# Kernel optimization log

Hardware: AMD Instinct MI355X
Metric: run time of the kernel (lower is better)

Reference implementation:

```python
import jax, jax.numpy as jnp
import numpy as np

SEQ, BATCH, D, N = 256, 4, 512, 32768
TEMP = 0.5


def setup_inputs() -> dict:
    key = jax.random.key(0)
    ks = jax.random.split(key, 16)
    d = D
    # xavier_uniform with gain 1/sqrt(2) for square [d,d]: limit = gain*sqrt(6/(d+d))
    lim_t = (1.0 / np.sqrt(2.0)) * np.sqrt(6.0 / (d + d))
    lim_g1 = np.sqrt(6.0 / (2 * d + d))  # default kaiming-ish scale approximated by xavier
    lim_g2 = np.sqrt(6.0 / (d + 1))
    inp = {
        "q": jax.random.normal(ks[0], (SEQ, BATCH, D), dtype=jnp.float32),
        "prev_layer_output": jax.random.normal(ks[1], (SEQ, BATCH, D), dtype=jnp.float32),
        "Wq": jax.random.uniform(ks[2], (D, D), jnp.float32, -lim_t, lim_t),
        "bq": jnp.zeros((D,), jnp.float32),
        "Wk": jax.random.uniform(ks[3], (D, D), jnp.float32, -lim_t, lim_t),
        "bk": jnp.zeros((D,), jnp.float32),
        "Wv": jax.random.uniform(ks[4], (D, D), jnp.float32, -lim_t, lim_t),
        "bv": jnp.zeros((D,), jnp.float32),
        "Wg1": jax.random.uniform(ks[5], (D, 2 * D), jnp.float32, -lim_g1, lim_g1),
        "bg1": jnp.zeros((D,), jnp.float32),
        "Wg2": jax.random.uniform(ks[6], (1, D), jnp.float32, -lim_g2, lim_g2),
        "bg2": jnp.zeros((1,), jnp.float32),
        "dstore_k": jax.random.normal(ks[7], (N, D), dtype=jnp.float32),
        "dstore_v": jax.random.normal(ks[8], (N, D), dtype=jnp.float32),
    }
    return inp


def reference(q, prev_layer_output, Wq, bq, Wk, bk, Wv, bv, Wg1, bg1, Wg2, bg2, dstore_k, dstore_v):
    # [S,B,D] -> [B,S,D]
    qb = jnp.transpose(q, (1, 0, 2))
    prevb = jnp.transpose(prev_layer_output, (1, 0, 2))
    # enable_tune projections
    _q = qb @ Wq.T + bq                      # [B,S,D]
    _k = dstore_k @ Wk.T + bk                # [N,D]
    _v = dstore_v @ Wv.T + bv                # [N,D]
    _q = _q * (D ** -0.5)
    # attention over datastore, temperature-scaled softmax
    logits = jnp.einsum("bsd,nd->bsn", _q, _k) / TEMP  # [B,S,N]
    w = jax.nn.softmax(logits, axis=-1)
    attn = jnp.einsum("bsn,nd->bsd", w, _v)            # [B,S,D]
    # gated residual fusion
    cat = jnp.concatenate([attn, prevb], axis=-1)      # [B,S,2D]
    h = jax.nn.relu(cat @ Wg1.T + bg1)                 # [B,S,D]
    sigma = jax.nn.sigmoid(h @ Wg2.T + bg2)            # [B,S,1]
    res = attn * sigma + prevb * (1.0 - sigma)
    return jnp.transpose(res, (1, 0, 2))               # [S,B,D]
```

## Files before the change

kernel.cpp:

```cpp
#include <hip/hip_runtime.h>
#include <hip/hip_bf16.h>
#include <cstdint>
#include <cstddef>


typedef unsigned short u16;
typedef u16    u16x8 __attribute__((ext_vector_type(8)));
typedef u16    u16x4 __attribute__((ext_vector_type(4)));
typedef __bf16 bf16x8 __attribute__((ext_vector_type(8)));
typedef float  f32x4 __attribute__((ext_vector_type(4)));

#define MFMA16(a, b, c) __builtin_amdgcn_mfma_f32_16x16x32_bf16( \
    __builtin_bit_cast(bf16x8, (a)), __builtin_bit_cast(bf16x8, (b)), (c), 0, 0, 0)

__device__ __forceinline__ u16 f2bf(float f) {
  unsigned u = __builtin_bit_cast(unsigned, f);
  u += 0x7fffu + ((u >> 16) & 1u);
  return (u16)(u >> 16);
}

__global__ __launch_bounds__(256) void prep_cvt(const float* __restrict__ src,
                                                u16* __restrict__ dst) {
  size_t i = ((size_t)blockIdx.x * 256 + threadIdx.x) * 4;
  float4 v = *(const float4*)(src + i);
  u16x4 o = {f2bf(v.x), f2bf(v.y), f2bf(v.z), f2bf(v.w)};
  *(u16x4*)(dst + i) = o;
}

__global__ __launch_bounds__(256) void prep_vt(const float* __restrict__ v,
                                               u16* __restrict__ vt) {
  __shared__ u16 Lt[64 * 72];
  const int n0 = blockIdx.x * 64, d0 = blockIdx.y * 64;
  const int t = threadIdx.x;
  const int n = t >> 2, c4 = t & 3;
#pragma unroll
  for (int i = 0; i < 4; i++) {
    int col = (c4 + 4 * i) * 4;
    float4 x = *(const float4*)(v + (size_t)(n0 + n) * 512 + d0 + col);
    Lt[(col + 0) * 72 + n] = f2bf(x.x);
    Lt[(col + 1) * 72 + n] = f2bf(x.y);
    Lt[(col + 2) * 72 + n] = f2bf(x.z);
    Lt[(col + 3) * 72 + n] = f2bf(x.w);
  }
  __syncthreads();
#pragma unroll
  for (int u = 0; u < 2; u++) {
    int unit = t + 256 * u;
    int d = unit >> 3, un = unit & 7;
    *(u16x8*)(vt + (size_t)(d0 + d) * 32768 + n0 + un * 8) =
        *(const u16x8*)&Lt[d * 72 + un * 8];
  }
}

template <bool TRANSB, bool CONCAT, bool RELU, bool OUTBF16, bool ROWSCALE>
__global__ __launch_bounds__(256, 2) void gemm64(
    const float* __restrict__ A, const float* __restrict__ A2,
    const float* __restrict__ B, const float* __restrict__ bias,
    const float* __restrict__ lvec, float alpha, void* __restrict__ Cv,
    int M, int N, int K) {
  __shared__ u16 As[64 * 72];
  __shared__ u16 Bs[64 * 72];
  const int tid = threadIdx.x;
  const int w = tid >> 6, lane = tid & 63, quad = lane >> 4, l15 = lane & 15;
  const int m0 = blockIdx.y * 64, n0 = blockIdx.x * 64;
  const int arow = tid >> 2, ac4 = tid & 3;
  float rs = 1.0f;
  if (ROWSCALE) rs = 1.0f / lvec[m0 + arow];
  const f32x4 fzero = {0.f, 0.f, 0.f, 0.f};
  f32x4 acc[4];
#pragma unroll
  for (int i = 0; i < 4; i++) acc[i] = fzero;

  for (int k0 = 0; k0 < K; k0 += 64) {
    __syncthreads();
    {
      const float* src;
      if (CONCAT)
        src = (k0 < 512) ? (A + (size_t)(m0 + arow) * 512 + k0)
                         : (A2 + (size_t)(m0 + arow) * 512 + (k0 - 512));
      else
        src = A + (size_t)(m0 + arow) * K + k0;
#pragma unroll
      for (int i = 0; i < 4; i++) {
        int col = (ac4 + 4 * i) * 4;
        float4 x = *(const float4*)(src + col);
        if (ROWSCALE) { x.x *= rs; x.y *= rs; x.z *= rs; x.w *= rs; }
        u16x4 o = {f2bf(x.x), f2bf(x.y), f2bf(x.z), f2bf(x.w)};
        *(u16x4*)&As[arow * 72 + col] = o;
      }
    }
    if (TRANSB) {
      const float* src = B + (size_t)(n0 + arow) * K + k0;
#pragma unroll
      for (int i = 0; i < 4; i++) {
        int col = (ac4 + 4 * i) * 4;
        float4 x = *(const float4*)(src + col);
        u16x4 o = {f2bf(x.x), f2bf(x.y), f2bf(x.z), f2bf(x.w)};
        *(u16x4*)&Bs[arow * 72 + col] = o;
      }
    } else {
      const float* src = B + (size_t)(k0 + arow) * N + n0;
#pragma unroll
      for (int i = 0; i < 4; i++) {
        int col = (ac4 + 4 * i) * 4;
        float4 x = *(const float4*)(src + col);
        Bs[(col + 0) * 72 + arow] = f2bf(x.x);
        Bs[(col + 1) * 72 + arow] = f2bf(x.y);
        Bs[(col + 2) * 72 + arow] = f2bf(x.z);
        Bs[(col + 3) * 72 + arow] = f2bf(x.w);
      }
    }
    __syncthreads();
#pragma unroll
    for (int ks = 0; ks < 2; ks++) {
      u16x8 af = *(const u16x8*)&As[(w * 16 + l15) * 72 + ks * 32 + quad * 8];
#pragma unroll
      for (int nt = 0; nt < 4; nt++) {
        u16x8 bf = *(const u16x8*)&Bs[(nt * 16 + l15) * 72 + ks * 32 + quad * 8];
        acc[nt] = MFMA16(af, bf, acc[nt]);
      }
    }
  }
#pragma unroll
  for (int nt = 0; nt < 4; nt++) {
    int col = n0 + nt * 16 + l15;
    float b = bias ? bias[col] : 0.f;
#pragma unroll
    for (int i = 0; i < 4; i++) {
      int row = m0 + w * 16 + quad * 4 + i;
      float y = (acc[nt][i] + b) * alpha;
      if (RELU) y = fmaxf(y, 0.f);
      if (OUTBF16)
        ((u16*)Cv)[(size_t)row * N + col] = f2bf(y);
      else
        ((float*)Cv)[(size_t)row * N + col] = y;
    }
  }
}

__global__ void cq_kernel(const float* __restrict__ q1,
                          const float* __restrict__ bk,
                          float* __restrict__ cq) {
  int r = blockIdx.x, lane = threadIdx.x;
  float s = 0.f;
#pragma unroll
  for (int k = 0; k < 512; k += 64) s += q1[(size_t)r * 512 + k + lane] * bk[k + lane];
#pragma unroll
  for (int off = 32; off; off >>= 1) s += __shfl_down(s, off, 64);
  if (lane == 0) cq[r] = 2.0f * s;
}

__global__ __launch_bounds__(512, 2) void flash(
    const u16* __restrict__ kbf,
    const u16* __restrict__ vt,
    const u16* __restrict__ q2,
    const float* __restrict__ cq,
    float* __restrict__ racc,
    float* __restrict__ lacc) {
  __shared__ u16 Ks[32 * 520];
  __shared__ u16 Es[64 * 40];
  const int tid = threadIdx.x;
  const int w = tid >> 6, lane = tid & 63, quad = lane >> 4, l15 = lane & 15;
  const int qt = blockIdx.x & 15, ch = blockIdx.x >> 4;
  const int qbase = qt * 64;
  const int qg = w >> 1, nh = w & 1;
  const int colb = w * 64;

  u16x8 qf[16];
  {
    const u16* qp = q2 + (size_t)(qbase + qg * 16 + l15) * 512 + quad * 8;
#pragma unroll
    for (int ks = 0; ks < 16; ks++) qf[ks] = *(const u16x8*)(qp + ks * 32);
  }
  float cq4[4];
#pragma unroll
  for (int i = 0; i < 4; i++) cq4[i] = cq[qbase + qg * 16 + quad * 4 + i];
  float lp[4] = {0.f, 0.f, 0.f, 0.f};
  const f32x4 fzero = {0.f, 0.f, 0.f, 0.f};
  f32x4 acc[4][4];
#pragma unroll
  for (int a = 0; a < 4; a++)
#pragma unroll
    for (int b = 0; b < 4; b++) acc[a][b] = fzero;

  u16x8 st[4];
  u16x8 bvp[4];
  int n0 = ch * 2048;
#pragma unroll
  for (int u = 0; u < 4; u++) {
    int flat = tid + u * 512;
    st[u] = *(const u16x8*)(kbf + (size_t)(n0 + (flat >> 6)) * 512 + (flat & 63) * 8);
  }
#pragma unroll
  for (int ct = 0; ct < 4; ct++)
    bvp[ct] = *(const u16x8*)(vt + (size_t)(colb + ct * 16 + l15) * 32768 + n0 + quad * 8);

#pragma unroll 1
  for (int sub = 0; sub < 64; ++sub) {
    n0 = ch * 2048 + sub * 32;
    __syncthreads();
#pragma unroll
    for (int u = 0; u < 4; u++) {
      int flat = tid + u * 512;
      *(u16x8*)&Ks[(flat >> 6) * 520 + (flat & 63) * 8] = st[u];
    }
    if (sub + 1 < 64) {
      int n1 = n0 + 32;
#pragma unroll
      for (int u = 0; u < 4; u++) {
        int flat = tid + u * 512;
        st[u] = *(const u16x8*)(kbf + (size_t)(n1 + (flat >> 6)) * 512 + (flat & 63) * 8);
      }
    }
    __syncthreads();
    f32x4 s = fzero;
#pragma unroll
    for (int ks = 0; ks < 16; ks++) {
      u16x8 bfg = *(const u16x8*)&Ks[(nh * 16 + l15) * 520 + ks * 32 + quad * 8];
      s = MFMA16(qf[ks], bfg, s);
    }
#pragma unroll
    for (int i = 0; i < 4; i++) {
      float e = __expf(s[i] + cq4[i]);
      lp[i] += e;
      Es[(qg * 16 + quad * 4 + i) * 40 + nh * 16 + l15] = f2bf(e);
    }
    __syncthreads();
    u16x8 ef[4];
#pragma unroll
    for (int q2i = 0; q2i < 4; q2i++)
      ef[q2i] = *(const u16x8*)&Es[(q2i * 16 + l15) * 40 + quad * 8];
#pragma unroll
    for (int ct = 0; ct < 4; ct++) {
#pragma unroll
      for (int q2i = 0; q2i < 4; q2i++)
        acc[q2i][ct] = MFMA16(ef[q2i], bvp[ct], acc[q2i][ct]);
    }
    if (sub + 1 < 64) {
      int n1 = n0 + 32;
#pragma unroll
      for (int ct = 0; ct < 4; ct++)
        bvp[ct] = *(const u16x8*)(vt + (size_t)(colb + ct * 16 + l15) * 32768 + n1 + quad * 8);
    }
  }
#pragma unroll
  for (int q2i = 0; q2i < 4; q2i++)
#pragma unroll
    for (int ct = 0; ct < 4; ct++) {
      int col = colb + ct * 16 + l15;
#pragma unroll
      for (int i = 0; i < 4; i++) {
        int row = qbase + q2i * 16 + quad * 4 + i;
        atomicAdd(&racc[(size_t)row * 512 + col], acc[q2i][ct][i]);
      }
    }
#pragma unroll
  for (int i = 0; i < 4; i++) {
    float v = lp[i];
#pragma unroll
    for (int off = 1; off < 16; off <<= 1) v += __shfl_xor(v, off, 64);
    if (l15 == 0) atomicAdd(&lacc[qbase + qg * 16 + quad * 4 + i], v);
  }
}

__global__ __launch_bounds__(256) void finalize(
    const float* __restrict__ h, const float* __restrict__ attn,
    const float* __restrict__ prev, const float* __restrict__ wg2,
    const float* __restrict__ bg2, float* __restrict__ out) {
  __shared__ float red[4];
  int r = blockIdx.x, t = threadIdx.x;
  const float* hr = h + (size_t)r * 512;
  float p = hr[t] * wg2[t] + hr[t + 256] * wg2[t + 256];
#pragma unroll
  for (int off = 32; off; off >>= 1) p += __shfl_down(p, off, 64);
  if ((t & 63) == 0) red[t >> 6] = p;
  __syncthreads();
  float dot = red[0] + red[1] + red[2] + red[3];
  float sg = 1.f / (1.f + __expf(-(dot + bg2[0])));
  size_t base = (size_t)r * 512;
  out[base + t] = attn[base + t] * sg + prev[base + t] * (1.f - sg);
  out[base + t + 256] = attn[base + t + 256] * sg + prev[base + t + 256] * (1.f - sg);
}

extern "C" void kernel_launch(void* const* d_in, const int* in_sizes, int n_in,
                              void* d_out, int out_size, void* d_ws, size_t ws_size,
                              hipStream_t stream) {
  const float* q    = (const float*)d_in[0];
  const float* prev = (const float*)d_in[1];
  const float* Wq   = (const float*)d_in[2];
  const float* bq   = (const float*)d_in[3];
  const float* Wk   = (const float*)d_in[4];
  const float* bk   = (const float*)d_in[5];
  const float* Wv   = (const float*)d_in[6];
  const float* bv   = (const float*)d_in[7];
  const float* Wg1  = (const float*)d_in[8];
  const float* bg1  = (const float*)d_in[9];
  const float* Wg2  = (const float*)d_in[10];
  const float* bg2  = (const float*)d_in[11];
  const float* dk   = (const float*)d_in[12];
  const float* dv   = (const float*)d_in[13];
  float* out = (float*)d_out;

  char* ws = (char*)d_ws;
  u16*   kbf  = (u16*)(ws);
  u16*   vt   = (u16*)(ws + 33554432);
  float* racc = (float*)(ws + 67108864);
  float* lacc = (float*)(ws + 69206016);
  float* cqv  = (float*)(ws + 69210112);
  u16*   q2   = (u16*)(ws + 69214208);
  float* q1   = (float*)(ws + 70262784);
  float* attn = (float*)(ws + 72359936);
  float* h    = q1;

  prep_cvt<<<16384, 256, 0, stream>>>(dk, kbf);
  prep_vt<<<dim3(512, 8), 256, 0, stream>>>(dv, vt);
  gemm64<true, false, false, false, false><<<dim3(8, 16), 256, 0, stream>>>(
      q, nullptr, Wq, bq, nullptr, 0.044194173824159216f, q1, 1024, 512, 512);
  cq_kernel<<<1024, 64, 0, stream>>>(q1, bk, cqv);
  gemm64<false, false, false, true, false><<<dim3(8, 16), 256, 0, stream>>>(
      q1, nullptr, Wk, nullptr, nullptr, 2.0f, q2, 1024, 512, 512);
  hipMemsetAsync(racc, 0, 2097152 + 4096, stream);
  flash<<<256, 512, 0, stream>>>(kbf, vt, q2, cqv, racc, lacc);
  gemm64<true, false, false, false, true><<<dim3(8, 16), 256, 0, stream>>>(
      racc, nullptr, Wv, bv, lacc, 1.0f, attn, 1024, 512, 512);
  gemm64<true, true, true, false, false><<<dim3(8, 16), 256, 0, stream>>>(
      attn, prev, Wg1, bg1, nullptr, 1.0f, h, 1024, 512, 1024);
  finalize<<<1024, 256, 0, stream>>>(h, attn, prev, Wg2, bg2, out);
}
```

Baseline: 419.4 us.

## Fuse cq and gate dot into GEMMs, pipeline flash PV, remap blocks per XCD

```diff
diff --git a/kernel.cpp b/kernel.cpp
--- a/kernel.cpp
+++ b/kernel.cpp
@@ -52,12 +52,14 @@
   }
 }
 
-template <bool TRANSB, bool CONCAT, bool RELU, bool OUTBF16, bool ROWSCALE>
+template <bool TRANSB, bool CONCAT, bool RELU, bool OUTBF16, bool ROWSCALE,
+          bool CQ, bool GATE, int KK>
 __global__ __launch_bounds__(256, 2) void gemm64(
     const float* __restrict__ A, const float* __restrict__ A2,
     const float* __restrict__ B, const float* __restrict__ bias,
-    const float* __restrict__ lvec, float alpha, void* __restrict__ Cv,
-    int M, int N, int K) {
+    const float* __restrict__ lvec, const float* __restrict__ bkv,
+    const float* __restrict__ wg2, float alpha, void* __restrict__ Cv,
+    float* __restrict__ cqout, float* __restrict__ sdot) {
   __shared__ u16 As[64 * 72];
   __shared__ u16 Bs[64 * 72];
   const int tid = threadIdx.x;
@@ -66,49 +68,64 @@
   const int arow = tid >> 2, ac4 = tid & 3;
   float rs = 1.0f;
   if (ROWSCALE) rs = 1.0f / lvec[m0 + arow];
+  const bool docq = CQ && (blockIdx.x == 0);
+  float cqacc = 0.f;
   const f32x4 fzero = {0.f, 0.f, 0.f, 0.f};
   f32x4 acc[4];
 #pragma unroll
   for (int i = 0; i < 4; i++) acc[i] = fzero;
 
-  for (int k0 = 0; k0 < K; k0 += 64) {
+  float4 ra[4], rb[4], rk[4];
+  auto loadA = [&](int k0) {
+    const float* src;
+    if (CONCAT)
+      src = (k0 < 512) ? (A + (size_t)(m0 + arow) * 512 + k0)
+                       : (A2 + (size_t)(m0 + arow) * 512 + (k0 - 512));
+    else
+      src = A + (size_t)(m0 + arow) * KK + k0;
+#pragma unroll
+    for (int i = 0; i < 4; i++) ra[i] = *(const float4*)(src + (ac4 + 4 * i) * 4);
+  };
+  auto loadB = [&](int k0) {
+    const float* src = TRANSB ? (B + (size_t)(n0 + arow) * KK + k0)
+                              : (B + (size_t)(k0 + arow) * 512 + n0);
+#pragma unroll
+    for (int i = 0; i < 4; i++) rb[i] = *(const float4*)(src + (ac4 + 4 * i) * 4);
+  };
+  auto loadK = [&](int k0) {
+#pragma unroll
+    for (int i = 0; i < 4; i++) rk[i] = *(const float4*)(bkv + k0 + (ac4 + 4 * i) * 4);
+  };
+
+  loadA(0); loadB(0);
+  if (docq) loadK(0);
+#pragma unroll
+  for (int k0 = 0; k0 < KK; k0 += 64) {
     __syncthreads();
-    {
-      const float* src;
-      if (CONCAT)
-        src = (k0 < 512) ? (A + (size_t)(m0 + arow) * 512 + k0)
-                         : (A2 + (size_t)(m0 + arow) * 512 + (k0 - 512));
-      else
-        src = A + (size_t)(m0 + arow) * K + k0;
-#pragma unroll
-      for (int i = 0; i < 4; i++) {
-        int col = (ac4 + 4 * i) * 4;
-        float4 x = *(const float4*)(src + col);
-        if (ROWSCALE) { x.x *= rs; x.y *= rs; x.z *= rs; x.w *= rs; }
-        u16x4 o = {f2bf(x.x), f2bf(x.y), f2bf(x.z), f2bf(x.w)};
-        *(u16x4*)&As[arow * 72 + col] = o;
-      }
-    }
-    if (TRANSB) {
-      const float* src = B + (size_t)(n0 + arow) * K + k0;
-#pragma unroll
-      for (int i = 0; i < 4; i++) {
-        int col = (ac4 + 4 * i) * 4;
-        float4 x = *(const float4*)(src + col);
-        u16x4 o = {f2bf(x.x), f2bf(x.y), f2bf(x.z), f2bf(x.w)};
-        *(u16x4*)&Bs[arow * 72 + col] = o;
-      }
-    } else {
-      const float* src = B + (size_t)(k0 + arow) * N + n0;
-#pragma unroll
-      for (int i = 0; i < 4; i++) {
-        int col = (ac4 + 4 * i) * 4;
-        float4 x = *(const float4*)(src + col);
-        Bs[(col + 0) * 72 + arow] = f2bf(x.x);
-        Bs[(col + 1) * 72 + arow] = f2bf(x.y);
-        Bs[(col + 2) * 72 + arow] = f2bf(x.z);
-        Bs[(col + 3) * 72 + arow] = f2bf(x.w);
-      }
+#pragma unroll
+    for (int i = 0; i < 4; i++) {
+      int col = (ac4 + 4 * i) * 4;
+      float4 x = ra[i];
+      if (ROWSCALE) { x.x *= rs; x.y *= rs; x.z *= rs; x.w *= rs; }
+      u16x4 oa = {f2bf(x.x), f2bf(x.y), f2bf(x.z), f2bf(x.w)};
+      *(u16x4*)&As[arow * 72 + col] = oa;
+      float4 y = rb[i];
+      if (TRANSB) {
+        u16x4 ob = {f2bf(y.x), f2bf(y.y), f2bf(y.z), f2bf(y.w)};
+        *(u16x4*)&Bs[arow * 72 + col] = ob;
+      } else {
+        Bs[(col + 0) * 72 + arow] = f2bf(y.x);
+        Bs[(col + 1) * 72 + arow] = f2bf(y.y);
+        Bs[(col + 2) * 72 + arow] = f2bf(y.z);
+        Bs[(col + 3) * 72 + arow] = f2bf(y.w);
+      }
+      if (docq)
+        cqacc += ra[i].x * rk[i].x + ra[i].y * rk[i].y + ra[i].z * rk[i].z +
+                 ra[i].w * rk[i].w;
+    }
+    if (k0 + 64 < KK) {
+      loadA(k0 + 64); loadB(k0 + 64);
+      if (docq) loadK(k0 + 64);
     }
     __syncthreads();
 #pragma unroll
@@ -121,33 +138,48 @@
       }
     }
   }
-#pragma unroll
-  for (int nt = 0; nt < 4; nt++) {
-    int col = n0 + nt * 16 + l15;
-    float b = bias ? bias[col] : 0.f;
+
+  if (docq) {
+    cqacc += __shfl_xor(cqacc, 1, 64);
+    cqacc += __shfl_xor(cqacc, 2, 64);
+    if (ac4 == 0) cqout[m0 + arow] = alpha * cqacc;
+  }
+  if (GATE) {
+    float part[4] = {0.f, 0.f, 0.f, 0.f};
+#pragma unroll
+    for (int nt = 0; nt < 4; nt++) {
+      int col = n0 + nt * 16 + l15;
+      float b = bias[col], wv = wg2[col];
+#pragma unroll
+      for (int i = 0; i < 4; i++) {
+        float y = fmaxf((acc[nt][i] + b) * alpha, 0.f);
+        part[i] += y * wv;
+      }
+    }
 #pragma unroll
     for (int i = 0; i < 4; i++) {
-      int row = m0 + w * 16 + quad * 4 + i;
-      float y = (acc[nt][i] + b) * alpha;
-      if (RELU) y = fmaxf(y, 0.f);
-      if (OUTBF16)
-        ((u16*)Cv)[(size_t)row * N + col] = f2bf(y);
-      else
-        ((float*)Cv)[(size_t)row * N + col] = y;
-    }
-  }
-}
-
-__global__ void cq_kernel(const float* __restrict__ q1,
-                          const float* __restrict__ bk,
-                          float* __restrict__ cq) {
-  int r = blockIdx.x, lane = threadIdx.x;
-  float s = 0.f;
-#pragma unroll
-  for (int k = 0; k < 512; k += 64) s += q1[(size_t)r * 512 + k + lane] * bk[k + lane];
-#pragma unroll
-  for (int off = 32; off; off >>= 1) s += __shfl_down(s, off, 64);
-  if (lane == 0) cq[r] = 2.0f * s;
+      float v = part[i];
+      v += __shfl_xor(v, 1, 64); v += __shfl_xor(v, 2, 64);
+      v += __shfl_xor(v, 4, 64); v += __shfl_xor(v, 8, 64);
+      if (l15 == 0) atomicAdd(&sdot[m0 + w * 16 + quad * 4 + i], v);
+    }
+  } else {
+#pragma unroll
+    for (int nt = 0; nt < 4; nt++) {
+      int col = n0 + nt * 16 + l15;
+      float b = bias ? bias[col] : 0.f;
+#pragma unroll
+      for (int i = 0; i < 4; i++) {
+        int row = m0 + w * 16 + quad * 4 + i;
+        float y = (acc[nt][i] + b) * alpha;
+        if (RELU) y = fmaxf(y, 0.f);
+        if (OUTBF16)
+          ((u16*)Cv)[(size_t)row * 512 + col] = f2bf(y);
+        else
+          ((float*)Cv)[(size_t)row * 512 + col] = y;
+      }
+    }
+  }
 }
 
 __global__ __launch_bounds__(512, 2) void flash(
@@ -158,10 +190,13 @@
     float* __restrict__ racc,
     float* __restrict__ lacc) {
   __shared__ u16 Ks[32 * 520];
-  __shared__ u16 Es[64 * 40];
+  __shared__ u16 Es[2][64 * 40];
   const int tid = threadIdx.x;
   const int w = tid >> 6, lane = tid & 63, quad = lane >> 4, l15 = lane & 15;
-  const int qt = blockIdx.x & 15, ch = blockIdx.x >> 4;
+  const int bx = blockIdx.x;
+  const int xcd = bx & 7, idx = bx >> 3;
+  const int qt = idx & 15, nh2 = idx >> 4;
+  const int rowbase = xcd * 4096 + nh2 * 2048;
   const int qbase = qt * 64;
   const int qg = w >> 1, nh = w & 1;
   const int colb = w * 64;
@@ -185,19 +220,15 @@
 
   u16x8 st[4];
   u16x8 bvp[4];
-  int n0 = ch * 2048;
 #pragma unroll
   for (int u = 0; u < 4; u++) {
     int flat = tid + u * 512;
-    st[u] = *(const u16x8*)(kbf + (size_t)(n0 + (flat >> 6)) * 512 + (flat & 63) * 8);
-  }
-#pragma unroll
-  for (int ct = 0; ct < 4; ct++)
-    bvp[ct] = *(const u16x8*)(vt + (size_t)(colb + ct * 16 + l15) * 32768 + n0 + quad * 8);
+    st[u] = *(const u16x8*)(kbf + (size_t)(rowbase + (flat >> 6)) * 512 + (flat & 63) * 8);
+  }
 
 #pragma unroll 1
   for (int sub = 0; sub < 64; ++sub) {
-    n0 = ch * 2048 + sub * 32;
+    const int n0 = rowbase + sub * 32;
     __syncthreads();
 #pragma unroll
     for (int u = 0; u < 4; u++) {
@@ -212,36 +243,48 @@
         st[u] = *(const u16x8*)(kbf + (size_t)(n1 + (flat >> 6)) * 512 + (flat & 63) * 8);
       }
     }
+    if (sub > 0) {
+      const u16* eb = Es[(sub - 1) & 1];
+      u16x8 ef[4];
+#pragma unroll
+      for (int q2i = 0; q2i < 4; q2i++)
+        ef[q2i] = *(const u16x8*)&eb[(q2i * 16 + l15) * 40 + quad * 8];
+#pragma unroll
+      for (int ct = 0; ct < 4; ct++)
+#pragma unroll
+        for (int q2i = 0; q2i < 4; q2i++)
+          acc[q2i][ct] = MFMA16(ef[q2i], bvp[ct], acc[q2i][ct]);
+    }
     __syncthreads();
+#pragma unroll
+    for (int ct = 0; ct < 4; ct++)
+      bvp[ct] = *(const u16x8*)(vt + (size_t)(colb + ct * 16 + l15) * 32768 + n0 + quad * 8);
     f32x4 s = fzero;
 #pragma unroll
     for (int ks = 0; ks < 16; ks++) {
       u16x8 bfg = *(const u16x8*)&Ks[(nh * 16 + l15) * 520 + ks * 32 + quad * 8];
       s = MFMA16(qf[ks], bfg, s);
     }
+    u16* ew = Es[sub & 1];
 #pragma unroll
     for (int i = 0; i < 4; i++) {
       float e = __expf(s[i] + cq4[i]);
       lp[i] += e;
-      Es[(qg * 16 + quad * 4 + i) * 40 + nh * 16 + l15] = f2bf(e);
-    }
-    __syncthreads();
+      ew[(qg * 16 + quad * 4 + i) * 40 + nh * 16 + l15] = f2bf(e);
+    }
+  }
+  __syncthreads();
+  {
+    const u16* eb = Es[1];
     u16x8 ef[4];
 #pragma unroll
     for (int q2i = 0; q2i < 4; q2i++)
-      ef[q2i] = *(const u16x8*)&Es[(q2i * 16 + l15) * 40 + quad * 8];
-#pragma unroll
-    for (int ct = 0; ct < 4; ct++) {
+      ef[q2i] = *(const u16x8*)&eb[(q2i * 16 + l15) * 40 + quad * 8];
+#pragma unroll
+    for (int ct = 0; ct < 4; ct++)
 #pragma unroll
       for (int q2i = 0; q2i < 4; q2i++)
         acc[q2i][ct] = MFMA16(ef[q2i], bvp[ct], acc[q2i][ct]);
-    }
-    if (sub + 1 < 64) {
-      int n1 = n0 + 32;
-#pragma unroll
-      for (int ct = 0; ct < 4; ct++)
-        bvp[ct] = *(const u16x8*)(vt + (size_t)(colb + ct * 16 + l15) * 32768 + n1 + quad * 8);
-    }
   }
 #pragma unroll
   for (int q2i = 0; q2i < 4; q2i++)
@@ -263,23 +306,17 @@
   }
 }
 
-__global__ __launch_bounds__(256) void finalize(
-    const float* __restrict__ h, const float* __restrict__ attn,
-    const float* __restrict__ prev, const float* __restrict__ wg2,
-    const float* __restrict__ bg2, float* __restrict__ out) {
-  __shared__ float red[4];
+__global__ __launch_bounds__(128) void finalize(
+    const float* __restrict__ sdot, const float* __restrict__ bg2,
+    const float* __restrict__ attn, const float* __restrict__ prev,
+    float* __restrict__ out) {
   int r = blockIdx.x, t = threadIdx.x;
-  const float* hr = h + (size_t)r * 512;
-  float p = hr[t] * wg2[t] + hr[t + 256] * wg2[t + 256];
-#pragma unroll
-  for (int off = 32; off; off >>= 1) p += __shfl_down(p, off, 64);
-  if ((t & 63) == 0) red[t >> 6] = p;
-  __syncthreads();
-  float dot = red[0] + red[1] + red[2] + red[3];
-  float sg = 1.f / (1.f + __expf(-(dot + bg2[0])));
-  size_t base = (size_t)r * 512;
-  out[base + t] = attn[base + t] * sg + prev[base + t] * (1.f - sg);
-  out[base + t + 256] = attn[base + t + 256] * sg + prev[base + t + 256] * (1.f - sg);
+  float sg = 1.f / (1.f + __expf(-(sdot[r] + bg2[0])));
+  float4 a = ((const float4*)(attn + (size_t)r * 512))[t];
+  float4 p = ((const float4*)(prev + (size_t)r * 512))[t];
+  float4 o = {a.x * sg + p.x * (1.f - sg), a.y * sg + p.y * (1.f - sg),
+              a.z * sg + p.z * (1.f - sg), a.w * sg + p.w * (1.f - sg)};
+  ((float4*)(out + (size_t)r * 512))[t] = o;
 }
 
 extern "C" void kernel_launch(void* const* d_in, const int* in_sizes, int n_in,
@@ -306,24 +343,28 @@
   u16*   vt   = (u16*)(ws + 33554432);
   float* racc = (float*)(ws + 67108864);
   float* lacc = (float*)(ws + 69206016);
-  float* cqv  = (float*)(ws + 69210112);
-  u16*   q2   = (u16*)(ws + 69214208);
-  float* q1   = (float*)(ws + 70262784);
-  float* attn = (float*)(ws + 72359936);
-  float* h    = q1;
+  float* sdot = (float*)(ws + 69210112);
+  float* cqv  = (float*)(ws + 69214208);
+  u16*   q2   = (u16*)(ws + 69218304);
+  float* q1   = (float*)(ws + 70266880);
+  float* attn = (float*)(ws + 72364032);
 
   prep_cvt<<<16384, 256, 0, stream>>>(dk, kbf);
   prep_vt<<<dim3(512, 8), 256, 0, stream>>>(dv, vt);
-  gemm64<true, false, false, false, false><<<dim3(8, 16), 256, 0, stream>>>(
-      q, nullptr, Wq, bq, nullptr, 0.044194173824159216f, q1, 1024, 512, 512);
-  cq_kernel<<<1024, 64, 0, stream>>>(q1, bk, cqv);
-  gemm64<false, false, false, true, false><<<dim3(8, 16), 256, 0, stream>>>(
-      q1, nullptr, Wk, nullptr, nullptr, 2.0f, q2, 1024, 512, 512);
-  hipMemsetAsync(racc, 0, 2097152 + 4096, stream);
+  gemm64<true, false, false, false, false, false, false, 512>
+      <<<dim3(8, 16), 256, 0, stream>>>(q, nullptr, Wq, bq, nullptr, nullptr,
+                                        nullptr, 0.044194173824159216f, q1,
+                                        nullptr, nullptr);
+  gemm64<false, false, false, true, false, true, false, 512>
+      <<<dim3(8, 16), 256, 0, stream>>>(q1, nullptr, Wk, nullptr, nullptr, bk,
+                                        nullptr, 2.0f, q2, cqv, nullptr);
+  hipMemsetAsync(racc, 0, 2105344, stream);
   flash<<<256, 512, 0, stream>>>(kbf, vt, q2, cqv, racc, lacc);
-  gemm64<true, false, false, false, true><<<dim3(8, 16), 256, 0, stream>>>(
-      racc, nullptr, Wv, bv, lacc, 1.0f, attn, 1024, 512, 512);
-  gemm64<true, true, true, false, false><<<dim3(8, 16), 256, 0, stream>>>(
-      attn, prev, Wg1, bg1, nullptr, 1.0f, h, 1024, 512, 1024);
-  finalize<<<1024, 256, 0, stream>>>(h, attn, prev, Wg2, bg2, out);
-}
+  gemm64<true, false, false, false, true, false, false, 512>
+      <<<dim3(8, 16), 256, 0, stream>>>(racc, nullptr, Wv, bv, lacc, nullptr,
+                                        nullptr, 1.0f, attn, nullptr, nullptr);
+  gemm64<true, true, true, false, false, false, true, 1024>
+      <<<dim3(8, 16), 256, 0, stream>>>(attn, prev, Wg1, bg1, nullptr, nullptr,
+                                        Wg2, 1.0f, nullptr, nullptr, sdot);
+  finalize<<<1024, 128, 0, stream>>>(sdot, bg2, attn, prev, out);
+}
```

After: 435.4 us. 3.8% more time.
